# Kernel tuning notes

Measured on AMD Instinct MI355X. Metric: run time of the kernel, lower is better.

Reference implementation:

```python
import jax, jax.numpy as jnp
import numpy as np

B, T, N, D = 64, 10, 64, 4      # batch, time steps, num_vars, input_size
H = 128                          # encoder_hidden
K = 2                            # num_edge_types
EPS = 1e-5                       # BatchNorm eps
_edges = np.ones((N, N)) - np.eye(N)
SEND = jnp.asarray(np.where(_edges)[0])   # [E], E = N*(N-1)
RECV = jnp.asarray(np.where(_edges)[1])   # [E]


def _xavier(key, shape):
    std = (2.0 / (shape[0] + shape[1])) ** 0.5
    return std * jax.random.normal(key, shape, dtype=jnp.float32)


def _mlp(x, w1, b1, w2, b2, g, beta):
    # RefNRIMLP: Linear -> ELU -> (dropout p=0) -> Linear -> ELU -> BatchNorm1d
    h = jax.nn.elu(x @ w1 + b1)
    h = jax.nn.elu(h @ w2 + b2)
    flat = h.reshape(-1, h.shape[-1])  # BN over flattened (batch*objects) axis
    mu = flat.mean(0)
    var = flat.var(0)
    flat = (flat - mu) * jax.lax.rsqrt(var + EPS) * g + beta
    return flat.reshape(h.shape)


def setup_inputs() -> dict:
    key = jax.random.key(0)
    ks = jax.random.split(key, 10)
    inp = {"inputs": jax.random.normal(ks[0], (B, T, N, D), dtype=jnp.float32)}
    fan_ins = {"mlp1": T * D, "mlp2": 2 * H, "mlp3": H, "mlp4": 3 * H}
    for i, (name, nin) in enumerate(fan_ins.items()):
        k1, k2 = jax.random.split(ks[i + 1])
        inp[name + "_w1"] = _xavier(k1, (nin, H))
        inp[name + "_b1"] = jnp.full((H,), 0.1, dtype=jnp.float32)
        inp[name + "_w2"] = _xavier(k2, (H, H))
        inp[name + "_b2"] = jnp.full((H,), 0.1, dtype=jnp.float32)
        inp[name + "_g"] = jnp.ones((H,), dtype=jnp.float32)
        inp[name + "_beta"] = jnp.zeros((H,), dtype=jnp.float32)
    inp["fc_w"] = _xavier(ks[9], (H, K))
    inp["fc_b"] = jnp.full((K,), 0.1, dtype=jnp.float32)
    return inp


def reference(inputs, mlp1_w1, mlp1_b1, mlp1_w2, mlp1_b2, mlp1_g, mlp1_beta,
              mlp2_w1, mlp2_b1, mlp2_w2, mlp2_b2, mlp2_g, mlp2_beta,
              mlp3_w1, mlp3_b1, mlp3_w2, mlp3_b2, mlp3_g, mlp3_beta,
              mlp4_w1, mlp4_b1, mlp4_w2, mlp4_b2, mlp4_g, mlp4_beta,
              fc_w, fc_b):
    # [B,T,N,D] -> [B,N,T*D]
    x = jnp.transpose(inputs, (0, 2, 1, 3)).reshape(B, N, T * D)
    x = _mlp(x, mlp1_w1, mlp1_b1, mlp1_w2, mlp1_b2, mlp1_g, mlp1_beta)
    # node2edge: gather send/recv node embeddings, concat -> [B,E,2H]
    x = jnp.concatenate([x[:, SEND], x[:, RECV]], axis=-1)
    x = _mlp(x, mlp2_w1, mlp2_b1, mlp2_w2, mlp2_b2, mlp2_g, mlp2_beta)
    x_skip = x
    # edge2node: one-hot(recv).T matmul == segment_sum over recv index, then /(N-1)
    agg = jax.ops.segment_sum(jnp.swapaxes(x, 0, 1), RECV, num_segments=N)  # [N,B,H]
    x = jnp.swapaxes(agg, 0, 1) / (N - 1)  # [B,N,H]
    x = _mlp(x, mlp3_w1, mlp3_b1, mlp3_w2, mlp3_b2, mlp3_g, mlp3_beta)
    x = jnp.concatenate([x[:, SEND], x[:, RECV]], axis=-1)  # [B,E,2H]
    x = jnp.concatenate([x, x_skip], axis=-1)  # [B,E,3H]
    x = _mlp(x, mlp4_w1, mlp4_b1, mlp4_w2, mlp4_b2, mlp4_g, mlp4_beta)
    return x @ fc_w + fc_b  # logits [B, E, K]
```

## Files before the change

kernel.cpp:

```cpp
#include <hip/hip_runtime.h>

#define BN_EPS 1e-5f

using h8 = __attribute__((ext_vector_type(8))) _Float16;
using h4v = __attribute__((ext_vector_type(4))) _Float16;
using f4v = __attribute__((ext_vector_type(4))) float;

#define OFF_COEF 0
#define OFF_CVEC 1024
#define OFF_H1 4096
#define OFF_P2 528384
#define OFF_Q2 1052672
#define OFF_H3 1576960
#define OFF_P4 2101248
#define OFF_Q4 2625536
#define OFF_W2P 3149824
#define OFF_W4P 3158016
#define OFF_WCP 3166208
#define OFF_H4B 3174400
#define WS_BYTES 78757888ull

__device__ __forceinline__ float elu_f(float x) {
    return x > 0.f ? x : __expf(x) - 1.f;
}


__device__ __forceinline__ void gemm32_globalW(const float* As, int lda,
                                               const float* __restrict__ Wg, int K,
                                               float acc[2][8], int tx, int ty) {
    const float4* Wg4 = (const float4*)Wg;
#pragma unroll 4
    for (int k = 0; k < K; ++k) {
        float a0 = As[ty * lda + k];
        float a1 = As[(ty + 16) * lda + k];
        float4 wa = Wg4[k * 32 + tx];
        float4 wb = Wg4[k * 32 + 16 + tx];
        const float wv[8] = {wa.x, wa.y, wa.z, wa.w, wb.x, wb.y, wb.z, wb.w};
#pragma unroll
        for (int u = 0; u < 8; ++u) {
            acc[0][u] = fmaf(a0, wv[u], acc[0][u]);
            acc[1][u] = fmaf(a1, wv[u], acc[1][u]);
        }
    }
}

__device__ __forceinline__ void gemm16_globalW(const float* As, int lda,
                                               const float* __restrict__ Wg, int K,
                                               float acc[8], int tx, int ty) {
    const float4* Wg4 = (const float4*)Wg;
#pragma unroll 4
    for (int k = 0; k < K; ++k) {
        float a0 = As[ty * lda + k];
        float4 wa = Wg4[k * 32 + tx];
        float4 wb = Wg4[k * 32 + 16 + tx];
        acc[0] = fmaf(a0, wa.x, acc[0]);
        acc[1] = fmaf(a0, wa.y, acc[1]);
        acc[2] = fmaf(a0, wa.z, acc[2]);
        acc[3] = fmaf(a0, wa.w, acc[3]);
        acc[4] = fmaf(a0, wb.x, acc[4]);
        acc[5] = fmaf(a0, wb.y, acc[5]);
        acc[6] = fmaf(a0, wb.z, acc[6]);
        acc[7] = fmaf(a0, wb.w, acc[7]);
    }
}

__device__ __forceinline__ void bias_elu32(const float acc[2][8],
                                           const float* __restrict__ bias,
                                           float vals[2][8], int tx) {
    int ca = 4 * tx, cb = 64 + 4 * tx;
    float bv[8] = {bias[ca], bias[ca + 1], bias[ca + 2], bias[ca + 3],
                   bias[cb], bias[cb + 1], bias[cb + 2], bias[cb + 3]};
#pragma unroll
    for (int j = 0; j < 2; ++j)
#pragma unroll
        for (int u = 0; u < 8; ++u)
            vals[j][u] = elu_f(acc[j][u] + bv[u]);
}

__device__ __forceinline__ void bias_elu16(const float acc[8],
                                           const float* __restrict__ bias,
                                           float vals[8], int tx) {
    int ca = 4 * tx, cb = 64 + 4 * tx;
    float bv[8] = {bias[ca], bias[ca + 1], bias[ca + 2], bias[ca + 3],
                   bias[cb], bias[cb + 1], bias[cb + 2], bias[cb + 3]};
#pragma unroll
    for (int u = 0; u < 8; ++u)
        vals[u] = elu_f(acc[u] + bv[u]);
}

__device__ __forceinline__ void store_tile32(float* __restrict__ out, int row0,
                                             const float vals[2][8], int tx, int ty) {
#pragma unroll
    for (int j = 0; j < 2; ++j) {
        int r = row0 + ty + 16 * j;
        *(float4*)(out + r * 128 + 4 * tx) =
            make_float4(vals[j][0], vals[j][1], vals[j][2], vals[j][3]);
        *(float4*)(out + r * 128 + 64 + 4 * tx) =
            make_float4(vals[j][4], vals[j][5], vals[j][6], vals[j][7]);
    }
}

__device__ __forceinline__ void stats_tail32_store(const float vals[2][8], float* red,
                                                   float* __restrict__ slot, int tid,
                                                   int tx, int ty) {
    float ls[8], lq[8];
#pragma unroll
    for (int u = 0; u < 8; ++u) {
        ls[u] = vals[0][u] + vals[1][u];
        lq[u] = vals[0][u] * vals[0][u] + vals[1][u] * vals[1][u];
    }
    __syncthreads();
    int ca = 4 * tx, cb = 64 + 4 * tx;
#pragma unroll
    for (int u = 0; u < 4; ++u) {
        red[ty * 128 + ca + u] = ls[u];
        red[2048 + ty * 128 + ca + u] = lq[u];
        red[ty * 128 + cb + u] = ls[u + 4];
        red[2048 + ty * 128 + cb + u] = lq[u + 4];
    }
    __syncthreads();
    if (tid < 128) {
        float s = 0.f, q = 0.f;
#pragma unroll
        for (int t = 0; t < 16; ++t) {
            s += red[t * 128 + tid];
            q += red[2048 + t * 128 + tid];
        }
        slot[tid] = s;
        slot[128 + tid] = q;
    }
}

__device__ __forceinline__ void stats_tail16_store(const float vals[8], float* red,
                                                   float* __restrict__ slot, int tid,
                                                   int tx, int ty) {
    __syncthreads();
    int ca = 4 * tx, cb = 64 + 4 * tx;
#pragma unroll
    for (int u = 0; u < 4; ++u) {
        red[ty * 128 + ca + u] = vals[u];
        red[2048 + ty * 128 + ca + u] = vals[u] * vals[u];
        red[ty * 128 + cb + u] = vals[u + 4];
        red[2048 + ty * 128 + cb + u] = vals[u + 4] * vals[u + 4];
    }
    __syncthreads();
    if (tid < 128) {
        float s = 0.f, q = 0.f;
#pragma unroll
        for (int t = 0; t < 16; ++t) {
            s += red[t * 128 + tid];
            q += red[2048 + t * 128 + tid];
        }
        slot[tid] = s;
        slot[128 + tid] = q;
    }
}


__device__ __forceinline__ void gemm1_swz(const _Float16* X,
                                          const _Float16* __restrict__ wp,
                                          f4v acc[4][2], int lane, int w,
                                          int cl, int quad) {
#pragma unroll
    for (int kc = 0; kc < 4; ++kc) {
        h8 bf0 = *(const h8*)&wp[(((w * 2 + 0) * 4 + kc) * 64 + lane) * 8];
        h8 bf1 = *(const h8*)&wp[(((w * 2 + 1) * 4 + kc) * 64 + lane) * 8];
        int co = ((kc * 4 + quad) ^ (cl & 7)) << 3;
        h8 af[4];
#pragma unroll
        for (int rt = 0; rt < 4; ++rt)
            af[rt] = *(const h8*)&X[(rt * 16 + cl) * 128 + co];
#pragma unroll
        for (int rt = 0; rt < 4; ++rt) {
            acc[rt][0] = __builtin_amdgcn_mfma_f32_16x16x32_f16(af[rt], bf0, acc[rt][0], 0, 0, 0);
            acc[rt][1] = __builtin_amdgcn_mfma_f32_16x16x32_f16(af[rt], bf1, acc[rt][1], 0, 0, 0);
        }
    }
}


__global__ __launch_bounds__(256) void k_mlp1p(const float* __restrict__ x,
                                               const float* __restrict__ w1,
                                               const float* __restrict__ b1,
                                               const float* __restrict__ w2,
                                               const float* __restrict__ b2,
                                               float* __restrict__ h1,
                                               float* __restrict__ slots,
                                               float* __restrict__ sums2,
                                               float* __restrict__ cvec,
                                               const float* __restrict__ w2src,
                                               _Float16* __restrict__ w2p,
                                               const float* __restrict__ w4src,
                                               _Float16* __restrict__ w4p) {
    __shared__ float Xs[32 * 44];
    __shared__ float As[32 * 132];
    int tid = threadIdx.x;
    int blk = blockIdx.x;
    if (blk >= 128) {
        if (blk < 193) {
            int i = (blk - 128) * 256 + tid;
            if (i < 16384) sums2[i] = 0.f;
            else if (i < 16512) cvec[i - 16384] = 0.f;
        } else {
            int second = blk >= 201;
            const float* src = second ? w4src : w2src;
            _Float16* wp = second ? w4p : w2p;
            int flat = (blk - (second ? 201 : 193)) * 256 + tid;
            int g = flat >> 6, L = flat & 63;
            int ct = g >> 2, kc = g & 3;
            int nn = ct * 16 + (L & 15), k0 = kc * 32 + (L >> 4) * 8;
            h8 v;
#pragma unroll
            for (int j = 0; j < 8; ++j) v[j] = (_Float16)src[(k0 + j) * 128 + nn];
            *(h8*)&wp[flat * 8] = v;
        }
        return;
    }
    int tx = tid & 15, ty = tid >> 4;
    int r0 = blk * 32;
    for (int idx = tid; idx < 32 * 40; idx += 256) {
        int r = idx / 40, k = idx - r * 40;
        int rr = r0 + r, b = rr >> 6, n = rr & 63, t = k >> 2, d = k & 3;
        Xs[r * 44 + k] = x[((b * 10 + t) * 64 + n) * 4 + d];
    }
    __syncthreads();
    float acc[2][8] = {};
    gemm32_globalW(Xs, 44, w1, 40, acc, tx, ty);
    float vals[2][8];
    bias_elu32(acc, b1, vals, tx);
    int ca = 4 * tx, cb = 64 + 4 * tx;
#pragma unroll
    for (int j = 0; j < 2; ++j) {
        int r = ty + 16 * j;
#pragma unroll
        for (int u = 0; u < 4; ++u) {
            As[r * 132 + ca + u] = vals[j][u];
            As[r * 132 + cb + u] = vals[j][u + 4];
        }
    }
    __syncthreads();
    float acc2[2][8] = {};
    gemm32_globalW(As, 132, w2, 128, acc2, tx, ty);
    float vals2[2][8];
    bias_elu32(acc2, b2, vals2, tx);
    store_tile32(h1, r0, vals2, tx, ty);
    stats_tail32_store(vals2, As, slots + blk * 256, tid, tx, ty);
}

__global__ __launch_bounds__(256) void k_pqf(const float* __restrict__ h,
                                             const float* __restrict__ slots,
                                             int nslots,
                                             const float* __restrict__ g,
                                             const float* __restrict__ beta,
                                             const float* __restrict__ w,
                                             float* __restrict__ P, float* __restrict__ Q,
                                             float* __restrict__ zero4) {
    __shared__ float Cf[256];
    __shared__ float As[16 * 132];
    int tid = threadIdx.x, tx = tid & 15, ty = tid >> 4;
    int half = blockIdx.x >> 8;
    int r0 = (blockIdx.x & 255) * 16;
    if (zero4 && tid < 32) zero4[blockIdx.x * 32 + tid] = 0.f;
    if (tid < 128) {
        int c = tid;
        float s = 0.f, q = 0.f;
#pragma unroll 8
        for (int t = 0; t < nslots; ++t) {
            s += slots[t * 256 + c];
            q += slots[t * 256 + 128 + c];
        }
        float mean = s * (1.f / 4096.f);
        float var = q * (1.f / 4096.f) - mean * mean;
        float a = g[c] * rsqrtf(var + BN_EPS);
        Cf[c] = a;
        Cf[128 + c] = beta[c] - mean * a;
    }
    __syncthreads();
    const float* Wg = w + half * 128 * 128;
    float* out = half ? Q : P;
    const float4* h4p = (const float4*)h;
#pragma unroll
    for (int i = 0; i < 2; ++i) {
        int f4 = tid + i * 256;
        int r = f4 >> 5, c4 = f4 & 31;
        float4 hv = h4p[(r0 + r) * 32 + c4];
        int cb = c4 * 4;
        float4 v;
        v.x = Cf[cb] * hv.x + Cf[128 + cb];
        v.y = Cf[cb + 1] * hv.y + Cf[128 + cb + 1];
        v.z = Cf[cb + 2] * hv.z + Cf[128 + cb + 2];
        v.w = Cf[cb + 3] * hv.w + Cf[128 + cb + 3];
        *(float4*)(As + r * 132 + c4 * 4) = v;
    }
    __syncthreads();
    float acc[8] = {};
    gemm16_globalW(As, 132, Wg, 128, acc, tx, ty);
    int r = r0 + ty;
    *(float4*)(out + r * 128 + 4 * tx) = make_float4(acc[0], acc[1], acc[2], acc[3]);
    *(float4*)(out + r * 128 + 64 + 4 * tx) = make_float4(acc[4], acc[5], acc[6], acc[7]);
}

__global__ __launch_bounds__(256, 6) void k_mlp2agg(const float* __restrict__ P2,
                                                    const float* __restrict__ Q2,
                                                    const float* __restrict__ b1,
                                                    const _Float16* __restrict__ w2p,
                                                    const float* __restrict__ b2,
                                                    float* __restrict__ aggraw,
                                                    _Float16* __restrict__ h2,
                                                    float* __restrict__ st) {
    __shared__ __align__(16) _Float16 Afr[9216];
    int tid = threadIdx.x;
    int lane = tid & 63, w = tid >> 6, cl = lane & 15, quad = lane >> 4;
    int b = blockIdx.x >> 6, n0 = blockIdx.x & 63;
    float* stc = st + n0 * 256;
    {
        int c4 = tid & 31;
        int rsub = tid >> 5;
        const float4* Qr = (const float4*)(Q2 + (b * 64 + n0) * 128);
        const float4* B1 = (const float4*)b1;
        float4 qv = Qr[c4];
        float4 bv = B1[c4];
        float qbx = qv.x + bv.x, qby = qv.y + bv.y;
        float qbz = qv.z + bv.z, qbw = qv.w + bv.w;
        const float4* P4p = (const float4*)(P2 + (size_t)b * 64 * 128);
#pragma unroll
        for (int it = 0; it < 8; ++it) {
            int r = it * 8 + rsub;
            int s0 = (r < 63) ? (r + (r >= n0 ? 1 : 0)) : n0;
            float4 p = P4p[s0 * 32 + c4];
            h4v v;
            v[0] = (_Float16)elu_f(p.x + qbx);
            v[1] = (_Float16)elu_f(p.y + qby);
            v[2] = (_Float16)elu_f(p.z + qbz);
            v[3] = (_Float16)elu_f(p.w + qbw);
            int off = r * 128 + ((((c4 >> 1) ^ (r & 7)) << 3) | ((c4 & 1) << 2));
            *(h4v*)&Afr[off] = v;
        }
    }
    __syncthreads();
    f4v acc[4][2];
#pragma unroll
    for (int rt = 0; rt < 4; ++rt)
#pragma unroll
        for (int c = 0; c < 2; ++c)
            acc[rt][c] = (f4v){0.f, 0.f, 0.f, 0.f};
    gemm1_swz(Afr, w2p, acc, lane, w, cl, quad);
    float v0[2][4][4];
#pragma unroll
    for (int ctl = 0; ctl < 2; ++ctl) {
        int col = (w * 2 + ctl) * 16 + cl;
        float bias = b2[col];
        float a0 = 0.f, sq = 0.f;
#pragma unroll
        for (int rt = 0; rt < 4; ++rt)
#pragma unroll
            for (int i = 0; i < 4; ++i) {
                int row = rt * 16 + quad * 4 + i;
                float va = elu_f(acc[rt][ctl][i] + bias);
                if (row == 63) va = 0.f;
                v0[ctl][rt][i] = va;
                a0 += va;
                sq += va * va;
            }
        a0 += __shfl_xor(a0, 16);
        sq += __shfl_xor(sq, 16);
        a0 += __shfl_xor(a0, 32);
        sq += __shfl_xor(sq, 32);
        if (quad == 0) {
            aggraw[(b * 64 + n0) * 128 + col] = a0;
            atomicAdd(stc + col, a0);
            atomicAdd(stc + 128 + col, sq);
        }
    }
    __syncthreads();
    unsigned short* T0 = (unsigned short*)Afr;
#pragma unroll
    for (int ctl = 0; ctl < 2; ++ctl) {
        int col = (w * 2 + ctl) * 16 + cl;
#pragma unroll
        for (int rt = 0; rt < 4; ++rt)
#pragma unroll
            for (int i = 0; i < 4; ++i) {
                int row = rt * 16 + quad * 4 + i;
                _Float16 ha = (_Float16)v0[ctl][rt][i];
                T0[row * 144 + col] = *(unsigned short*)&ha;
            }
    }
    __syncthreads();
    {
        int rr = tid >> 2, cq = tid & 3;
        if (rr < 63) {
            int s0 = rr + (rr >= n0 ? 1 : 0);
            int e0 = s0 * 63 + (s0 > n0 ? n0 : n0 - 1);
            unsigned short* d0 = (unsigned short*)h2 + ((size_t)b * 4032 + e0) * 128;
#pragma unroll
            for (int i = 0; i < 4; ++i) {
                int off = i * 32 + cq * 8;
                *(uint4*)(d0 + off) = *(uint4*)&T0[rr * 144 + off];
            }
        }
    }
}

__global__ __launch_bounds__(128) void k_wcfin(const float* __restrict__ sums2,
                                               const float* __restrict__ g2,
                                               const float* __restrict__ be2,
                                               const float* __restrict__ w41,
                                               _Float16* __restrict__ wcp,
                                               float* __restrict__ cvec,
                                               float* __restrict__ coef2) {
    __shared__ float red[128];
    __shared__ float pr[2];
    int k = blockIdx.x, c = threadIdx.x;
    red[c] = (c < 64) ? sums2[c * 256 + k] : sums2[(c - 64) * 256 + 128 + k];
    __syncthreads();
    if (c == 0) {
        float s = 0.f, q = 0.f;
#pragma unroll 8
        for (int t = 0; t < 64; ++t) {
            s += red[t];
            q += red[64 + t];
        }
        float mean = s * (1.f / 258048.f);
        float var = q * (1.f / 258048.f) - mean * mean;
        float a = g2[k] * rsqrtf(var + BN_EPS);
        pr[0] = a;
        pr[1] = be2[k] - mean * a;
        coef2[k] = a;
        coef2[128 + k] = pr[1];
    }
    __syncthreads();
    float a2k = pr[0], sh2k = pr[1];
    float wv = w41[(256 + k) * 128 + c];
    int g = (c >> 4) * 4 + (k >> 5);
    int L = ((k >> 3) & 3) * 16 + (c & 15);
    int j = k & 7;
    wcp[(g * 64 + L) * 8 + j] = (_Float16)(a2k * wv);
    atomicAdd(&cvec[c], sh2k * wv);
}

__global__ __launch_bounds__(256) void k_mlp3(const float* __restrict__ raw,
                                              const float* __restrict__ coef2,
                                              const float* __restrict__ w1,
                                              const float* __restrict__ b1,
                                              const float* __restrict__ w2,
                                              const float* __restrict__ b2,
                                              float* __restrict__ h3,
                                              float* __restrict__ slots) {
    __shared__ float As[4224];
    int tid = threadIdx.x, tx = tid & 15, ty = tid >> 4;
    int r0 = blockIdx.x * 16;
    const float4* in4 = (const float4*)raw;
    const float4* av = (const float4*)coef2;
    const float4* cv = (const float4*)(coef2 + 128);
    const float inv63 = 1.f / 63.f;
#pragma unroll
    for (int i = 0; i < 2; ++i) {
        int f4 = tid + i * 256;
        int r = f4 >> 5, c4 = f4 & 31;
        float4 hv = in4[(r0 + r) * 32 + c4];
        float4 a = av[c4], c = cv[c4];
        float4 v;
        v.x = a.x * hv.x * inv63 + c.x;
        v.y = a.y * hv.y * inv63 + c.y;
        v.z = a.z * hv.z * inv63 + c.z;
        v.w = a.w * hv.w * inv63 + c.w;
        *(float4*)(As + r * 132 + c4 * 4) = v;
    }
    __syncthreads();
    float acc[8] = {};
    gemm16_globalW(As, 132, w1, 128, acc, tx, ty);
    float vals[8];
    bias_elu16(acc, b1, vals, tx);
    __syncthreads();
    int ca = 4 * tx, cb = 64 + 4 * tx;
#pragma unroll
    for (int u = 0; u < 4; ++u) {
        As[ty * 132 + ca + u] = vals[u];
        As[ty * 132 + cb + u] = vals[u + 4];
    }
    __syncthreads();
    float acc2[8] = {};
    gemm16_globalW(As, 132, w2, 128, acc2, tx, ty);
    float vals2[8];
    bias_elu16(acc2, b2, vals2, tx);
    int r = r0 + ty;
    *(float4*)(h3 + r * 128 + 4 * tx) = make_float4(vals2[0], vals2[1], vals2[2], vals2[3]);
    *(float4*)(h3 + r * 128 + 64 + 4 * tx) = make_float4(vals2[4], vals2[5], vals2[6], vals2[7]);
    stats_tail16_store(vals2, As, slots + blockIdx.x * 256, tid, tx, ty);
}

__global__ __launch_bounds__(256, 6) void k_mlp4r3(const _Float16* __restrict__ h2,
                                                   const float* __restrict__ P4,
                                                   const float* __restrict__ Q4,
                                                   const _Float16* __restrict__ wcp,
                                                   const float* __restrict__ cvec,
                                                   const float* __restrict__ b1,
                                                   const _Float16* __restrict__ w4p2,
                                                   const float* __restrict__ b2,
                                                   unsigned short* __restrict__ h4,
                                                   float* __restrict__ st) {
    __shared__ __align__(16) _Float16 Afr[8192];
    int tid = threadIdx.x;
    int lane = tid & 63, w = tid >> 6, cl = lane & 15, quad = lane >> 4;
    unsigned t0 = blockIdx.x;
    unsigned b0 = t0 / 63;
    unsigned e00 = (t0 - b0 * 63) * 64;
    float* stc = st + (blockIdx.x & 63) * 256;
    {
        const _Float16* hb = h2 + (size_t)t0 * 8192;
#pragma unroll
        for (int i = 0; i < 4; ++i) {
            int u = tid + i * 256;
            int r = u >> 4, c = u & 15;
            h8 v = *(const h8*)&hb[r * 128 + c * 8];
            *(h8*)&Afr[r * 128 + ((c ^ (r & 7)) << 3)] = v;
        }
    }
    __syncthreads();
    f4v acc[4][2];
#pragma unroll
    for (int rt = 0; rt < 4; ++rt)
#pragma unroll
        for (int c = 0; c < 2; ++c)
            acc[rt][c] = (f4v){0.f, 0.f, 0.f, 0.f};
    gemm1_swz(Afr, wcp, acc, lane, w, cl, quad);
    float v0[4][2][4];
    {
        int col0 = w * 32 + cl, col1 = col0 + 16;
        float base0 = b1[col0] + cvec[col0];
        float base1 = b1[col1] + cvec[col1];
        unsigned sA0 = e00 / 63;
        unsigned baseE0 = sA0 * 63;
        unsigned eB0 = baseE0 + 63;
        unsigned sB0 = sA0 < 63u ? sA0 + 1u : sA0;
        const float* PA0 = P4 + (b0 * 64 + sA0) * 128;
        const float* PB0 = P4 + (b0 * 64 + sB0) * 128;
        float pA0c0 = PA0[col0], pA0c1 = PA0[col1];
        float pB0c0 = PB0[col0], pB0c1 = PB0[col1];
        const float* Qb0 = Q4 + (size_t)b0 * 8192;
#pragma unroll
        for (int rt = 0; rt < 4; ++rt)
#pragma unroll
            for (int i = 0; i < 4; ++i) {
                int rr = rt * 16 + quad * 4 + i;
                unsigned e = e00 + rr;
                bool hi = e >= eB0;
                unsigned s = hi ? sB0 : sA0;
                unsigned jj = e - (hi ? eB0 : baseE0);
                unsigned rv = jj + (jj >= s ? 1u : 0u);
                const float* Qr = Qb0 + rv * 128;
                float p0 = hi ? pB0c0 : pA0c0, p1 = hi ? pB0c1 : pA0c1;
                v0[rt][0][i] = elu_f(acc[rt][0][i] + p0 + Qr[col0] + base0);
                v0[rt][1][i] = elu_f(acc[rt][1][i] + p1 + Qr[col1] + base1);
            }
    }
    __syncthreads();
    {
        int colb0 = w * 32 + cl, colb1 = colb0 + 16;
        int cc0 = colb0 >> 3, cj0 = colb0 & 7;
        int cc1 = colb1 >> 3, cj1 = colb1 & 7;
#pragma unroll
        for (int rt = 0; rt < 4; ++rt)
#pragma unroll
            for (int i = 0; i < 4; ++i) {
                int row = rt * 16 + quad * 4 + i;
                int rx = row & 7;
                Afr[row * 128 + (((cc0 ^ rx) << 3) | cj0)] = (_Float16)v0[rt][0][i];
                Afr[row * 128 + (((cc1 ^ rx) << 3) | cj1)] = (_Float16)v0[rt][1][i];
            }
    }
    __syncthreads();
#pragma unroll
    for (int rt = 0; rt < 4; ++rt)
#pragma unroll
        for (int c = 0; c < 2; ++c)
            acc[rt][c] = (f4v){0.f, 0.f, 0.f, 0.f};
    gemm1_swz(Afr, w4p2, acc, lane, w, cl, quad);
#pragma unroll
    for (int ctl = 0; ctl < 2; ++ctl) {
        int col = (w * 2 + ctl) * 16 + cl;
        float bias = b2[col];
        float s1 = 0.f, s2 = 0.f;
#pragma unroll
        for (int rt = 0; rt < 4; ++rt)
#pragma unroll
            for (int i = 0; i < 4; ++i) {
                float va = elu_f(acc[rt][ctl][i] + bias);
                v0[rt][ctl][i] = va;
                s1 += va;
                s2 += va * va;
            }
        s1 += __shfl_xor(s1, 16);
        s2 += __shfl_xor(s2, 16);
        s1 += __shfl_xor(s1, 32);
        s2 += __shfl_xor(s2, 32);
        if (quad == 0) {
            atomicAdd(stc + col, s1);
            atomicAdd(stc + 128 + col, s2);
        }
    }
    {
        unsigned short* o0 = h4 + (size_t)t0 * 8192;
#pragma unroll
        for (int ctl = 0; ctl < 2; ++ctl) {
            int cg = w * 2 + ctl;
#pragma unroll
            for (int rt = 0; rt < 4; ++rt) {
                int idx = ((cg * 4 + rt) * 4 + quad) * 64 + cl * 4;
                h4v a;
#pragma unroll
                for (int i = 0; i < 4; ++i) a[i] = (_Float16)v0[rt][ctl][i];
                *(h4v*)(o0 + idx) = a;
            }
        }
    }
}

__global__ __launch_bounds__(256) void k_outf(const unsigned short* __restrict__ h4,
                                              const float* __restrict__ sums4,
                                              const float* __restrict__ g4,
                                              const float* __restrict__ be4,
                                              const float* __restrict__ fcw,
                                              const float* __restrict__ fcb,
                                              float* __restrict__ out) {
    __shared__ float U0[128];
    __shared__ float U1[128];
    __shared__ float Cp[4];
    int tid = threadIdx.x;
    if (tid < 128) {
        int c = tid;
        float s = 0.f, q = 0.f;
#pragma unroll 8
        for (int t = 0; t < 64; ++t) {
            s += sums4[t * 256 + c];
            q += sums4[t * 256 + 128 + c];
        }
        float mean = s * (1.f / 258048.f);
        float var = q * (1.f / 258048.f) - mean * mean;
        float a = g4[c] * rsqrtf(var + BN_EPS);
        float sh = be4[c] - mean * a;
        float w0 = fcw[2 * c], w1 = fcw[2 * c + 1];
        U0[c] = a * w0;
        U1[c] = a * w1;
        float p0 = sh * w0, p1 = sh * w1;
#pragma unroll
        for (int off = 1; off < 64; off <<= 1) {
            p0 += __shfl_xor(p0, off);
            p1 += __shfl_xor(p1, off);
        }
        if ((tid & 63) == 0) {
            Cp[(tid >> 6) * 2] = p0;
            Cp[(tid >> 6) * 2 + 1] = p1;
        }
    }
    __syncthreads();
    float C0 = Cp[0] + Cp[2] + fcb[0];
    float C1 = Cp[1] + Cp[3] + fcb[1];
    int lane = tid & 63, w = tid >> 6;
    int quad = lane >> 4, cl = lane & 15;
    float u0r[8], u1r[8];
#pragma unroll
    for (int cg = 0; cg < 8; ++cg) {
        u0r[cg] = U0[cg * 16 + cl];
        u1r[cg] = U1[cg * 16 + cl];
    }
    size_t tile = (size_t)blockIdx.x * 4 + w;
    const unsigned short* hb = h4 + tile * 8192;
#pragma unroll
    for (int rt = 0; rt < 4; ++rt) {
        float s00 = 0.f, s01 = 0.f, s02 = 0.f, s03 = 0.f;
        float s10 = 0.f, s11 = 0.f, s12 = 0.f, s13 = 0.f;
#pragma unroll
        for (int cg = 0; cg < 8; ++cg) {
            h4v hv = *(const h4v*)(hb + ((cg * 4 + rt) * 4 + quad) * 64 + cl * 4);
            float u0 = u0r[cg], u1 = u1r[cg];
            float x0 = (float)hv[0], x1 = (float)hv[1];
            float x2 = (float)hv[2], x3 = (float)hv[3];
            s00 = fmaf(x0, u0, s00); s01 = fmaf(x1, u0, s01);
            s02 = fmaf(x2, u0, s02); s03 = fmaf(x3, u0, s03);
            s10 = fmaf(x0, u1, s10); s11 = fmaf(x1, u1, s11);
            s12 = fmaf(x2, u1, s12); s13 = fmaf(x3, u1, s13);
        }
#pragma unroll
        for (int off = 1; off < 16; off <<= 1) {
            s00 += __shfl_xor(s00, off); s01 += __shfl_xor(s01, off);
            s02 += __shfl_xor(s02, off); s03 += __shfl_xor(s03, off);
            s10 += __shfl_xor(s10, off); s11 += __shfl_xor(s11, off);
            s12 += __shfl_xor(s12, off); s13 += __shfl_xor(s13, off);
        }
        if (cl == 0) {
            size_t R = tile * 64 + rt * 16 + quad * 4;
            *(float4*)(out + R * 2) =
                make_float4(s00 + C0, s10 + C1, s01 + C0, s11 + C1);
            *(float4*)(out + R * 2 + 4) =
                make_float4(s02 + C0, s12 + C1, s03 + C0, s13 + C1);
        }
    }
}


extern "C" void kernel_launch(void* const* d_in, const int* in_sizes, int n_in,
                              void* d_out, int out_size, void* d_ws, size_t ws_size,
                              hipStream_t stream) {
    const float* x = (const float*)d_in[0];
    const float* m1_w1 = (const float*)d_in[1];
    const float* m1_b1 = (const float*)d_in[2];
    const float* m1_w2 = (const float*)d_in[3];
    const float* m1_b2 = (const float*)d_in[4];
    const float* m1_g = (const float*)d_in[5];
    const float* m1_be = (const float*)d_in[6];
    const float* m2_w1 = (const float*)d_in[7];
    const float* m2_b1 = (const float*)d_in[8];
    const float* m2_w2 = (const float*)d_in[9];
    const float* m2_b2 = (const float*)d_in[10];
    const float* m2_g = (const float*)d_in[11];
    const float* m2_be = (const float*)d_in[12];
    const float* m3_w1 = (const float*)d_in[13];
    const float* m3_b1 = (const float*)d_in[14];
    const float* m3_w2 = (const float*)d_in[15];
    const float* m3_b2 = (const float*)d_in[16];
    const float* m3_g = (const float*)d_in[17];
    const float* m3_be = (const float*)d_in[18];
    const float* m4_w1 = (const float*)d_in[19];
    const float* m4_b1 = (const float*)d_in[20];
    const float* m4_w2 = (const float*)d_in[21];
    const float* m4_b2 = (const float*)d_in[22];
    const float* m4_g = (const float*)d_in[23];
    const float* m4_be = (const float*)d_in[24];
    const float* fc_w = (const float*)d_in[25];
    const float* fc_b = (const float*)d_in[26];
    float* out = (float*)d_out;

    float* W = (float*)d_ws;
    float* coef2 = W + OFF_COEF;
    float* cvec = W + OFF_CVEC;
    float* h1 = W + OFF_H1;
    float* aggraw = h1;
    float* sums4 = h1;
    float* P2 = W + OFF_P2;
    float* sums3 = P2;
    float* Q2 = W + OFF_Q2;
    float* h3 = W + OFF_H3;
    float* sums1 = h3;
    float* P4 = W + OFF_P4;
    float* sums2 = P4;
    float* Q4 = W + OFF_Q4;
    _Float16* w2p2 = (_Float16*)(W + OFF_W2P);
    _Float16* w4p2 = (_Float16*)(W + OFF_W4P);
    _Float16* wcp = (_Float16*)(W + OFF_WCP);
    _Float16* h2f = (_Float16*)(W + OFF_H4B);
    unsigned short* h4b = (unsigned short*)(W + OFF_H4B);

    if (ws_size < WS_BYTES) return;

    k_mlp1p<<<209, 256, 0, stream>>>(x, m1_w1, m1_b1, m1_w2, m1_b2, h1, sums1,
                                     sums2, cvec, m2_w2, w2p2, m4_w2, w4p2);
    k_pqf<<<512, 256, 0, stream>>>(h1, sums1, 128, m1_g, m1_be, m2_w1, P2, Q2, nullptr);
    k_mlp2agg<<<4096, 256, 0, stream>>>(P2, Q2, m2_b1, w2p2, m2_b2, aggraw, h2f, sums2);
    k_wcfin<<<128, 128, 0, stream>>>(sums2, m2_g, m2_be, m4_w1, wcp, cvec, coef2);
    k_mlp3<<<256, 256, 0, stream>>>(aggraw, coef2, m3_w1, m3_b1, m3_w2, m3_b2, h3, sums3);
    k_pqf<<<512, 256, 0, stream>>>(h3, sums3, 256, m3_g, m3_be, m4_w1, P4, Q4, sums4);
    k_mlp4r3<<<4032, 256, 0, stream>>>(h2f, P4, Q4, wcp, cvec, m4_b1, w4p2, m4_b2,
                                       h4b, sums4);
    k_outf<<<1008, 256, 0, stream>>>(h4b, sums4, m4_g, m4_be, fc_w, fc_b, out);
}
```

Measured before the change: 284.3 us.

## Split mlp1 into 16-row tiles, reorder mlp4 gather before MFMA, relax occupancy

The first MLP kernel now processes 16 rows per block instead of 32. This doubles its grid to 256 compute blocks (plus the auxiliary zeroing and weight-packing blocks) and the number of BN stat slots that the next kernel reduces. In the mlp4 kernel the P/Q gather plus bias is computed before the MFMA GEMM and ELU is applied afterwards, so global-load latency can overlap the tensor work. The launch-bounds occupancy hint drops from 6 to 5 waves, giving the compiler more registers to hold the extra live values.

```diff
diff --git a/kernel.cpp b/kernel.cpp
--- a/kernel.cpp
+++ b/kernel.cpp
@@ -24,25 +24,6 @@
     return x > 0.f ? x : __expf(x) - 1.f;
 }
 
-
-__device__ __forceinline__ void gemm32_globalW(const float* As, int lda,
-                                               const float* __restrict__ Wg, int K,
-                                               float acc[2][8], int tx, int ty) {
-    const float4* Wg4 = (const float4*)Wg;
-#pragma unroll 4
-    for (int k = 0; k < K; ++k) {
-        float a0 = As[ty * lda + k];
-        float a1 = As[(ty + 16) * lda + k];
-        float4 wa = Wg4[k * 32 + tx];
-        float4 wb = Wg4[k * 32 + 16 + tx];
-        const float wv[8] = {wa.x, wa.y, wa.z, wa.w, wb.x, wb.y, wb.z, wb.w};
-#pragma unroll
-        for (int u = 0; u < 8; ++u) {
-            acc[0][u] = fmaf(a0, wv[u], acc[0][u]);
-            acc[1][u] = fmaf(a1, wv[u], acc[1][u]);
-        }
-    }
-}
 
 __device__ __forceinline__ void gemm16_globalW(const float* As, int lda,
                                                const float* __restrict__ Wg, int K,
@@ -64,19 +45,6 @@
     }
 }
 
-__device__ __forceinline__ void bias_elu32(const float acc[2][8],
-                                           const float* __restrict__ bias,
-                                           float vals[2][8], int tx) {
-    int ca = 4 * tx, cb = 64 + 4 * tx;
-    float bv[8] = {bias[ca], bias[ca + 1], bias[ca + 2], bias[ca + 3],
-                   bias[cb], bias[cb + 1], bias[cb + 2], bias[cb + 3]};
-#pragma unroll
-    for (int j = 0; j < 2; ++j)
-#pragma unroll
-        for (int u = 0; u < 8; ++u)
-            vals[j][u] = elu_f(acc[j][u] + bv[u]);
-}
-
 __device__ __forceinline__ void bias_elu16(const float acc[8],
                                            const float* __restrict__ bias,
                                            float vals[8], int tx) {
@@ -86,49 +54,6 @@
 #pragma unroll
     for (int u = 0; u < 8; ++u)
         vals[u] = elu_f(acc[u] + bv[u]);
-}
-
-__device__ __forceinline__ void store_tile32(float* __restrict__ out, int row0,
-                                             const float vals[2][8], int tx, int ty) {
-#pragma unroll
-    for (int j = 0; j < 2; ++j) {
-        int r = row0 + ty + 16 * j;
-        *(float4*)(out + r * 128 + 4 * tx) =
-            make_float4(vals[j][0], vals[j][1], vals[j][2], vals[j][3]);
-        *(float4*)(out + r * 128 + 64 + 4 * tx) =
-            make_float4(vals[j][4], vals[j][5], vals[j][6], vals[j][7]);
-    }
-}
-
-__device__ __forceinline__ void stats_tail32_store(const float vals[2][8], float* red,
-                                                   float* __restrict__ slot, int tid,
-                                                   int tx, int ty) {
-    float ls[8], lq[8];
-#pragma unroll
-    for (int u = 0; u < 8; ++u) {
-        ls[u] = vals[0][u] + vals[1][u];
-        lq[u] = vals[0][u] * vals[0][u] + vals[1][u] * vals[1][u];
-    }
-    __syncthreads();
-    int ca = 4 * tx, cb = 64 + 4 * tx;
-#pragma unroll
-    for (int u = 0; u < 4; ++u) {
-        red[ty * 128 + ca + u] = ls[u];
-        red[2048 + ty * 128 + ca + u] = lq[u];
-        red[ty * 128 + cb + u] = ls[u + 4];
-        red[2048 + ty * 128 + cb + u] = lq[u + 4];
-    }
-    __syncthreads();
-    if (tid < 128) {
-        float s = 0.f, q = 0.f;
-#pragma unroll
-        for (int t = 0; t < 16; ++t) {
-            s += red[t * 128 + tid];
-            q += red[2048 + t * 128 + tid];
-        }
-        slot[tid] = s;
-        slot[128 + tid] = q;
-    }
 }
 
 __device__ __forceinline__ void stats_tail16_store(const float vals[8], float* red,
@@ -192,20 +117,20 @@
                                                _Float16* __restrict__ w2p,
                                                const float* __restrict__ w4src,
                                                _Float16* __restrict__ w4p) {
-    __shared__ float Xs[32 * 44];
-    __shared__ float As[32 * 132];
+    __shared__ float Xs[16 * 44];
+    __shared__ float As[4224];
     int tid = threadIdx.x;
     int blk = blockIdx.x;
-    if (blk >= 128) {
-        if (blk < 193) {
-            int i = (blk - 128) * 256 + tid;
+    if (blk >= 256) {
+        if (blk < 321) {
+            int i = (blk - 256) * 256 + tid;
             if (i < 16384) sums2[i] = 0.f;
             else if (i < 16512) cvec[i - 16384] = 0.f;
         } else {
-            int second = blk >= 201;
+            int second = blk >= 329;
             const float* src = second ? w4src : w2src;
             _Float16* wp = second ? w4p : w2p;
-            int flat = (blk - (second ? 201 : 193)) * 256 + tid;
+            int flat = (blk - (second ? 329 : 321)) * 256 + tid;
             int g = flat >> 6, L = flat & 63;
             int ct = g >> 2, kc = g & 3;
             int nn = ct * 16 + (L & 15), k0 = kc * 32 + (L >> 4) * 8;
@@ -217,34 +142,32 @@
         return;
     }
     int tx = tid & 15, ty = tid >> 4;
-    int r0 = blk * 32;
-    for (int idx = tid; idx < 32 * 40; idx += 256) {
+    int r0 = blk * 16;
+    for (int idx = tid; idx < 16 * 40; idx += 256) {
         int r = idx / 40, k = idx - r * 40;
         int rr = r0 + r, b = rr >> 6, n = rr & 63, t = k >> 2, d = k & 3;
         Xs[r * 44 + k] = x[((b * 10 + t) * 64 + n) * 4 + d];
     }
     __syncthreads();
-    float acc[2][8] = {};
-    gemm32_globalW(Xs, 44, w1, 40, acc, tx, ty);
-    float vals[2][8];
-    bias_elu32(acc, b1, vals, tx);
+    float acc[8] = {};
+    gemm16_globalW(Xs, 44, w1, 40, acc, tx, ty);
+    float vals[8];
+    bias_elu16(acc, b1, vals, tx);
     int ca = 4 * tx, cb = 64 + 4 * tx;
 #pragma unroll
-    for (int j = 0; j < 2; ++j) {
-        int r = ty + 16 * j;
-#pragma unroll
-        for (int u = 0; u < 4; ++u) {
-            As[r * 132 + ca + u] = vals[j][u];
-            As[r * 132 + cb + u] = vals[j][u + 4];
-        }
-    }
-    __syncthreads();
-    float acc2[2][8] = {};
-    gemm32_globalW(As, 132, w2, 128, acc2, tx, ty);
-    float vals2[2][8];
-    bias_elu32(acc2, b2, vals2, tx);
-    store_tile32(h1, r0, vals2, tx, ty);
-    stats_tail32_store(vals2, As, slots + blk * 256, tid, tx, ty);
+    for (int u = 0; u < 4; ++u) {
+        As[ty * 132 + ca + u] = vals[u];
+        As[ty * 132 + cb + u] = vals[u + 4];
+    }
+    __syncthreads();
+    float acc2[8] = {};
+    gemm16_globalW(As, 132, w2, 128, acc2, tx, ty);
+    float vals2[8];
+    bias_elu16(acc2, b2, vals2, tx);
+    int r = r0 + ty;
+    *(float4*)(h1 + r * 128 + 4 * tx) = make_float4(vals2[0], vals2[1], vals2[2], vals2[3]);
+    *(float4*)(h1 + r * 128 + 64 + 4 * tx) = make_float4(vals2[4], vals2[5], vals2[6], vals2[7]);
+    stats_tail16_store(vals2, As, slots + blk * 256, tid, tx, ty);
 }
 
 __global__ __launch_bounds__(256) void k_pqf(const float* __restrict__ h,
@@ -490,7 +413,7 @@
     stats_tail16_store(vals2, As, slots + blockIdx.x * 256, tid, tx, ty);
 }
 
-__global__ __launch_bounds__(256, 6) void k_mlp4r3(const _Float16* __restrict__ h2,
+__global__ __launch_bounds__(256, 5) void k_mlp4r3(const _Float16* __restrict__ h2,
                                                    const float* __restrict__ P4,
                                                    const float* __restrict__ Q4,
                                                    const _Float16* __restrict__ wcp,
@@ -517,14 +440,6 @@
             *(h8*)&Afr[r * 128 + ((c ^ (r & 7)) << 3)] = v;
         }
     }
-    __syncthreads();
-    f4v acc[4][2];
-#pragma unroll
-    for (int rt = 0; rt < 4; ++rt)
-#pragma unroll
-        for (int c = 0; c < 2; ++c)
-            acc[rt][c] = (f4v){0.f, 0.f, 0.f, 0.f};
-    gemm1_swz(Afr, wcp, acc, lane, w, cl, quad);
     float v0[4][2][4];
     {
         int col0 = w * 32 + cl, col1 = col0 + 16;
@@ -551,10 +466,25 @@
                 unsigned rv = jj + (jj >= s ? 1u : 0u);
                 const float* Qr = Qb0 + rv * 128;
                 float p0 = hi ? pB0c0 : pA0c0, p1 = hi ? pB0c1 : pA0c1;
-                v0[rt][0][i] = elu_f(acc[rt][0][i] + p0 + Qr[col0] + base0);
-                v0[rt][1][i] = elu_f(acc[rt][1][i] + p1 + Qr[col1] + base1);
+                v0[rt][0][i] = p0 + Qr[col0] + base0;
+                v0[rt][1][i] = p1 + Qr[col1] + base1;
             }
     }
+    __syncthreads();
+    f4v acc[4][2];
+#pragma unroll
+    for (int rt = 0; rt < 4; ++rt)
+#pragma unroll
+        for (int c = 0; c < 2; ++c)
+            acc[rt][c] = (f4v){0.f, 0.f, 0.f, 0.f};
+    gemm1_swz(Afr, wcp, acc, lane, w, cl, quad);
+#pragma unroll
+    for (int rt = 0; rt < 4; ++rt)
+#pragma unroll
+        for (int i = 0; i < 4; ++i) {
+            v0[rt][0][i] = elu_f(acc[rt][0][i] + v0[rt][0][i]);
+            v0[rt][1][i] = elu_f(acc[rt][1][i] + v0[rt][1][i]);
+        }
     __syncthreads();
     {
         int colb0 = w * 32 + cl, colb1 = colb0 + 16;
@@ -754,9 +684,9 @@
 
     if (ws_size < WS_BYTES) return;
 
-    k_mlp1p<<<209, 256, 0, stream>>>(x, m1_w1, m1_b1, m1_w2, m1_b2, h1, sums1,
+    k_mlp1p<<<337, 256, 0, stream>>>(x, m1_w1, m1_b1, m1_w2, m1_b2, h1, sums1,
                                      sums2, cvec, m2_w2, w2p2, m4_w2, w4p2);
-    k_pqf<<<512, 256, 0, stream>>>(h1, sums1, 128, m1_g, m1_be, m2_w1, P2, Q2, nullptr);
+    k_pqf<<<512, 256, 0, stream>>>(h1, sums1, 256, m1_g, m1_be, m2_w1, P2, Q2, nullptr);
     k_mlp2agg<<<4096, 256, 0, stream>>>(P2, Q2, m2_b1, w2p2, m2_b2, aggraw, h2f, sums2);
     k_wcfin<<<128, 128, 0, stream>>>(sums2, m2_g, m2_be, m4_w1, wcp, cvec, coef2);
     k_mlp3<<<256, 256, 0, stream>>>(aggraw, coef2, m3_w1, m3_b1, m3_w2, m3_b2, h3, sums3);
```

After: 302.6 us. 6.4% more time.
